# Kernel tuning notes

Hardware: AMD Instinct MI355X
Metric: run time of the kernel (lower is better)

## Reference

```python
import jax, jax.numpy as jnp
import numpy as np

B = 64        # number of bags
D = 512       # feature dim
T = 131072    # total instances across all bags (ragged, avg ~2048/bag)


def setup_inputs() -> dict:
    key = jax.random.key(0)
    k_s, _ = jax.random.split(key)
    samples = jax.random.normal(k_s, (T, D), dtype=jnp.float32)
    # Ragged bag sizes that sum exactly to T (deterministic).
    rng = np.random.default_rng(0)
    w = rng.random(B)
    counts = np.floor(w / w.sum() * T).astype(np.int64)
    counts = np.maximum(counts, 1)
    counts[-1] += T - counts.sum()
    bags_num_samples = jnp.asarray(counts, dtype=jnp.int64)
    return {"samples": samples, "bags_num_samples": bags_num_samples}


def reference(samples, bags_num_samples):
    # Fused segmented mean-pool replacing the per-bag Python loop:
    # bag i owns rows [cum[i-1], cum[i]) of `samples`.
    n_bags = bags_num_samples.shape[0]
    total = samples.shape[0]
    seg_ids = jnp.repeat(jnp.arange(n_bags), bags_num_samples,
                         total_repeat_length=total)  # [T]
    sums = jax.ops.segment_sum(samples, seg_ids, num_segments=n_bags)  # [B, D]
    return sums / bags_num_samples[:, None].astype(samples.dtype)
```

## Files before the change

kernel.cpp:

```cpp
#include <hip/hip_runtime.h>

#define NBAGS 64
#define D 512
#define D4 128
#define TARGET_CHUNKS 1024
#define GRID1 1088


__device__ __forceinline__ int lane_incl_scan(int v, int lane) {
#pragma unroll
    for (int off = 1; off < 64; off <<= 1) {
        int o = __shfl_up(v, off, 64);
        if (lane >= off) v += o;
    }
    return v;
}

__global__ __launch_bounds__(256) void
agg_fused_kernel(const float* __restrict__ samples,
                 const int* __restrict__ counts,
                 float* __restrict__ out, int tt) {
    __shared__ int s_bag, s_r0, s_r1, s_cnt;
    const int t = threadIdx.x;
    const int g = blockIdx.x;

    if (t == 0) s_bag = -1;
    if (t < 64) {
        const int c = counts[t];
        int n = (c * TARGET_CHUNKS) / tt;
        if (n < 1) n = 1;
        int S = n;
#pragma unroll
        for (int m = 1; m < 64; m <<= 1) S += __shfl_xor(S, m, 64);
        int L = TARGET_CHUNKS - S; if (L < 0) L = 0;
        n += (t < L) ? 1 : 0;
        const int cb = lane_incl_scan(n, t) - n;
        const int rb = lane_incl_scan(c, t) - c;
        if (g >= cb && g < cb + n) {
            const int j = g - cb;
            s_bag = t;
            s_cnt = c;
            s_r0 = rb + (c * j) / n;
            s_r1 = rb + (c * (j + 1)) / n;
        }
    }
    __syncthreads();
    if (s_bag < 0) return;
    const int r0 = s_r0, r1 = s_r1;

    const int col  = t & (D4 - 1);
    const int half = t >> 7;

    const float4* __restrict__ src = (const float4*)samples;

    float4 a0 = make_float4(0.f, 0.f, 0.f, 0.f);
    float4 a1 = make_float4(0.f, 0.f, 0.f, 0.f);
    int r = r0 + half;
    for (; r + 6 < r1; r += 8) {
        float4 v0 = src[(r    ) * D4 + col];
        float4 v1 = src[(r + 2) * D4 + col];
        float4 v2 = src[(r + 4) * D4 + col];
        float4 v3 = src[(r + 6) * D4 + col];
        a0.x += v0.x; a0.y += v0.y; a0.z += v0.z; a0.w += v0.w;
        a1.x += v1.x; a1.y += v1.y; a1.z += v1.z; a1.w += v1.w;
        a0.x += v2.x; a0.y += v2.y; a0.z += v2.z; a0.w += v2.w;
        a1.x += v3.x; a1.y += v3.y; a1.z += v3.z; a1.w += v3.w;
    }
    for (; r < r1; r += 2) {
        float4 v = src[r * D4 + col];
        a0.x += v.x; a0.y += v.y; a0.z += v.z; a0.w += v.w;
    }
    a0.x += a1.x; a0.y += a1.y; a0.z += a1.z; a0.w += a1.w;

    __shared__ float4 lds[D4];
    if (half == 1) lds[col] = a0;
    __syncthreads();
    if (half == 0) {
        float4 o = lds[col];
        a0.x += o.x; a0.y += o.y; a0.z += o.z; a0.w += o.w;
        const float inv = 1.0f / (float)s_cnt;
        float* dst = out + s_bag * D + col * 4;
        atomicAdd(dst + 0, a0.x * inv);
        atomicAdd(dst + 1, a0.y * inv);
        atomicAdd(dst + 2, a0.z * inv);
        atomicAdd(dst + 3, a0.w * inv);
    }
}

extern "C" void kernel_launch(void* const* d_in, const int* in_sizes, int n_in,
                              void* d_out, int out_size, void* d_ws, size_t ws_size,
                              hipStream_t stream) {
    const float* samples = (const float*)d_in[0];
    const int*   counts  = (const int*)d_in[1];
    float*       out     = (float*)d_out;
    const int    tt      = in_sizes[0] / D;

    hipMemsetAsync(out, 0, (size_t)out_size * sizeof(float), stream);
    agg_fused_kernel<<<GRID1, 256, 0, stream>>>(samples, counts, out, tt);
}
```

Measured before the change: 54.00 us.

## Split rows into equal slabs per block with bag-boundary walking

Replaces per-bag proportional chunk assignment with a fixed split of all rows into 1024 equal slabs, one per block. Each block binary-searches the bag prefix sum to find its starting bag and loops over bag segments inside its slab, emitting atomics per segment. This evens out per-block work and removes the 64 idle blocks of the old grid, at the cost of extra syncs and atomics where a slab crosses a bag boundary.

```diff
diff --git a/kernel.cpp b/kernel.cpp
--- a/kernel.cpp
+++ b/kernel.cpp
@@ -3,8 +3,7 @@
 #define NBAGS 64
 #define D 512
 #define D4 128
-#define TARGET_CHUNKS 1024
-#define GRID1 1088
+#define NCH 1024
 
 
 __device__ __forceinline__ int lane_incl_scan(int v, int lane) {
@@ -17,73 +16,78 @@
 }
 
 __global__ __launch_bounds__(256) void
-agg_fused_kernel(const float* __restrict__ samples,
-                 const int* __restrict__ counts,
-                 float* __restrict__ out, int tt) {
-    __shared__ int s_bag, s_r0, s_r1, s_cnt;
+agg_slab_kernel(const float* __restrict__ samples,
+                const int* __restrict__ counts,
+                float* __restrict__ out, int tt) {
+    __shared__ int s_ps[NBAGS + 1];
+    __shared__ float4 s_red[D4];
+
     const int t = threadIdx.x;
     const int g = blockIdx.x;
 
-    if (t == 0) s_bag = -1;
+    if (t == 0) s_ps[0] = 0;
     if (t < 64) {
         const int c = counts[t];
-        int n = (c * TARGET_CHUNKS) / tt;
-        if (n < 1) n = 1;
-        int S = n;
-#pragma unroll
-        for (int m = 1; m < 64; m <<= 1) S += __shfl_xor(S, m, 64);
-        int L = TARGET_CHUNKS - S; if (L < 0) L = 0;
-        n += (t < L) ? 1 : 0;
-        const int cb = lane_incl_scan(n, t) - n;
-        const int rb = lane_incl_scan(c, t) - c;
-        if (g >= cb && g < cb + n) {
-            const int j = g - cb;
-            s_bag = t;
-            s_cnt = c;
-            s_r0 = rb + (c * j) / n;
-            s_r1 = rb + (c * (j + 1)) / n;
-        }
+        s_ps[t + 1] = lane_incl_scan(c, t);
     }
     __syncthreads();
-    if (s_bag < 0) return;
-    const int r0 = s_r0, r1 = s_r1;
+
+    const int r0 = (int)(((long long)g * tt) / NCH);
+    const int r1 = (int)(((long long)(g + 1) * tt) / NCH);
 
     const int col  = t & (D4 - 1);
     const int half = t >> 7;
-
     const float4* __restrict__ src = (const float4*)samples;
 
-    float4 a0 = make_float4(0.f, 0.f, 0.f, 0.f);
-    float4 a1 = make_float4(0.f, 0.f, 0.f, 0.f);
-    int r = r0 + half;
-    for (; r + 6 < r1; r += 8) {
-        float4 v0 = src[(r    ) * D4 + col];
-        float4 v1 = src[(r + 2) * D4 + col];
-        float4 v2 = src[(r + 4) * D4 + col];
-        float4 v3 = src[(r + 6) * D4 + col];
-        a0.x += v0.x; a0.y += v0.y; a0.z += v0.z; a0.w += v0.w;
-        a1.x += v1.x; a1.y += v1.y; a1.z += v1.z; a1.w += v1.w;
-        a0.x += v2.x; a0.y += v2.y; a0.z += v2.z; a0.w += v2.w;
-        a1.x += v3.x; a1.y += v3.y; a1.z += v3.z; a1.w += v3.w;
+    int k;
+    {
+        int lo = 0, hi = NBAGS;
+        while (hi - lo > 1) {
+            int mid = (lo + hi) >> 1;
+            if (s_ps[mid] <= r0) lo = mid; else hi = mid;
+        }
+        k = lo;
     }
-    for (; r < r1; r += 2) {
-        float4 v = src[r * D4 + col];
-        a0.x += v.x; a0.y += v.y; a0.z += v.z; a0.w += v.w;
-    }
-    a0.x += a1.x; a0.y += a1.y; a0.z += a1.z; a0.w += a1.w;
 
-    __shared__ float4 lds[D4];
-    if (half == 1) lds[col] = a0;
-    __syncthreads();
-    if (half == 0) {
-        float4 o = lds[col];
-        a0.x += o.x; a0.y += o.y; a0.z += o.z; a0.w += o.w;
-        const float inv = 1.0f / (float)s_cnt;
-        float* dst = out + s_bag * D + col * 4;
-        atomicAdd(dst + 0, a0.x * inv);
-        atomicAdd(dst + 1, a0.y * inv);
-        atomicAdd(dst + 2, a0.z * inv);
-        atomicAdd(dst + 3, a0.w * inv);
+    int cur = r0;
+    while (cur < r1) {
+        const int bend = s_ps[k + 1];
+        const int e    = (bend < r1) ? bend : r1;
+
+        float4 a0 = make_float4(0.f, 0.f, 0.f, 0.f);
+        float4 a1 = make_float4(0.f, 0.f, 0.f, 0.f);
+        int r = cur + half;
+        for (; r + 6 < e; r += 8) {
+            float4 v0 = src[(r    ) * D4 + col];
+            float4 v1 = src[(r + 2) * D4 + col];
+            float4 v2 = src[(r + 4) * D4 + col];
+            float4 v3 = src[(r + 6) * D4 + col];
+            a0.x += v0.x; a0.y += v0.y; a0.z += v0.z; a0.w += v0.w;
+            a1.x += v1.x; a1.y += v1.y; a1.z += v1.z; a1.w += v1.w;
+            a0.x += v2.x; a0.y += v2.y; a0.z += v2.z; a0.w += v2.w;
+            a1.x += v3.x; a1.y += v3.y; a1.z += v3.z; a1.w += v3.w;
+        }
+        for (; r < e; r += 2) {
+            float4 v = src[r * D4 + col];
+            a0.x += v.x; a0.y += v.y; a0.z += v.z; a0.w += v.w;
+        }
+        a0.x += a1.x; a0.y += a1.y; a0.z += a1.z; a0.w += a1.w;
+
+        if (half == 1) s_red[col] = a0;
+        __syncthreads();
+        if (half == 0) {
+            float4 o = s_red[col];
+            a0.x += o.x; a0.y += o.y; a0.z += o.z; a0.w += o.w;
+            const float inv = 1.0f / (float)(s_ps[k + 1] - s_ps[k]);
+            float* dst = out + k * D + col * 4;
+            atomicAdd(dst + 0, a0.x * inv);
+            atomicAdd(dst + 1, a0.y * inv);
+            atomicAdd(dst + 2, a0.z * inv);
+            atomicAdd(dst + 3, a0.w * inv);
+        }
+        __syncthreads();
+        cur = e;
+        ++k;
     }
 }
 
@@ -96,5 +100,5 @@
     const int    tt      = in_sizes[0] / D;
 
     hipMemsetAsync(out, 0, (size_t)out_size * sizeof(float), stream);
-    agg_fused_kernel<<<GRID1, 256, 0, stream>>>(samples, counts, out, tt);
+    agg_slab_kernel<<<NCH, 256, 0, stream>>>(samples, counts, out, tt);
 }
```

Result: faster. 52.15 us (-3.4%).
